# Kernel tuning notes

Measured on AMD Instinct MI355X. Metric: run time of the kernel, lower is better.

Reference implementation:

```python
import jax, jax.numpy as jnp
import numpy as np

N_HID = 18  # hardcoded hidden width in the original module


def setup_inputs() -> dict:
    key = jax.random.key(0)
    ks = jax.random.split(key, 9)
    B, NODES, F = 262144, 5, 6
    scale = 0.1
    return {
        "x": jax.random.normal(ks[0], (B, NODES, F), dtype=jnp.float32),
        "Wf": jax.random.normal(ks[1], (F, N_HID), dtype=jnp.float32) * scale,
        "bf": jnp.zeros((N_HID,), dtype=jnp.float32),
        "Wm": jax.random.normal(ks[2], (2 * N_HID, N_HID), dtype=jnp.float32) * scale,
        "bm": jnp.zeros((N_HID,), dtype=jnp.float32),
        "Wu": jax.random.normal(ks[3], (3 * N_HID, N_HID), dtype=jnp.float32) * scale,
        "bu": jnp.zeros((N_HID,), dtype=jnp.float32),
        "Wr": jax.random.normal(ks[4], (5 * N_HID, 1), dtype=jnp.float32) * scale,
        "br": jnp.zeros((1,), dtype=jnp.float32),
    }


def reference(x, Wf, bf, Wm, bm, Wu, bu, Wr, br):
    # Node feature embedding: [B,5,F] -> [B,5,18]
    h = jnp.tanh(jnp.einsum("bnf,fh->bnh", x, Wf) + bf)
    U = h  # Ua..Ue initialized to a..e
    # Ring edges (a,b),(b,c),(c,d),(d,e),(e,a): pair each node with next node
    m_in = jnp.concatenate([U, jnp.roll(U, -1, axis=1)], axis=2)  # [B,5,36]
    M = jnp.tanh(jnp.einsum("bne,eh->bnh", m_in, Wm) + bm)  # edge i = (node i, node i+1)
    # Node i is updated with message from edge (i-1, i) -> roll messages by +1
    u_in = jnp.concatenate([jnp.roll(M, 1, axis=1), U, h], axis=2)  # [B,5,54]
    U = jnp.tanh(jnp.einsum("bne,eh->bnh", u_in, Wu) + bu)
    # Readout: concat Ua..Ue -> [B,90] -> [B,1]
    flat = U.reshape(U.shape[0], 5 * N_HID)
    return flat @ Wr + br
```

## Files before the change

kernel.cpp:

```cpp
#include <hip/hip_runtime.h>
#include <stdint.h>


#define NH 18
#define PSTR 68
#define NPL 99

typedef _Float16 half8 __attribute__((ext_vector_type(8)));
typedef float float4v __attribute__((ext_vector_type(4)));
union AB { uint32_t u[4]; half8 v; };

__device__ __forceinline__ float fast_tanh(float x) {
    float t = __builtin_amdgcn_exp2f(x * 2.8853900817779268f);
    float r = __builtin_amdgcn_rcpf(t + 1.0f);
    return __builtin_fmaf(-2.0f, r, 1.0f);
}
__device__ __forceinline__ uint32_t pkh(float a, float b) {
    union { _Float16 h[2]; uint32_t u; } z;
    z.h[0] = (_Float16)a; z.h[1] = (_Float16)b; return z.u;
}

#define MFMA16(A, Bv, Cv) __builtin_amdgcn_mfma_f32_16x16x32_f16((A).v, (Bv).v, (Cv), 0, 0, 0)

__global__ __launch_bounds__(256, 4) void mp_mfma(
    const float* __restrict__ x,
    const float* __restrict__ Wf, const float* __restrict__ bf,
    const float* __restrict__ Wm, const float* __restrict__ bm,
    const float* __restrict__ Wu, const float* __restrict__ bu,
    const float* __restrict__ Wr, const float* __restrict__ br,
    float* __restrict__ out, int B)
{
    __shared__ uint32_t lds[NPL * PSTR];
    const int tid = threadIdx.x;
    const int lane = tid & 63, w = tid >> 6;
    const int l15 = lane & 15, q = lane >> 4;

    for (int v = tid; v < 640; v += 256) {
        const int fi = v >> 6, ln = v & 63;
        const int fq = ln >> 4, fl = ln & 15;
        int rt, ks, which;
        if (fi < 2)      { which = 0; rt = fi;            ks = 0; }
        else if (fi < 6) { which = 1; rt = (fi - 2) >> 1; ks = (fi - 2) & 1; }
        else             { which = 2; rt = (fi - 6) >> 1; ks = (fi - 6) & 1; }
        const int m = rt * 16 + fl;
        for (int jp = 0; jp < 4; ++jp) {
            float vv[2];
            for (int hh = 0; hh < 2; ++hh) {
                int k = ks * 32 + fq * 8 + jp * 2 + hh;
                float val = 0.0f;
                if (m < NH) {
                    if (which == 0) {
                        if (k < 6) val = Wf[k * NH + m];
                        else if (k == 6) val = bf[m];
                    } else if (which == 1) {
                        if (k < 36) val = Wm[k * NH + m];
                        else if (k == 36) val = bm[m];
                    } else {
                        if (k < NH) val = Wu[k * NH + m];
                        else if (k < 36) val = Wu[k * NH + m] + Wu[(k + NH) * NH + m];
                        else if (k == 36) val = bu[m];
                    }
                }
                vv[hh] = val;
            }
            lds[fi * 256 + ln * 4 + jp] = pkh(vv[0], vv[1]);
        }
    }
    __syncthreads();
    AB F[10];
    #pragma unroll
    for (int f = 0; f < 10; ++f) {
        const int o = f * 256 + lane * 4;
        F[f].u[0] = lds[o];     F[f].u[1] = lds[o + 1];
        F[f].u[2] = lds[o + 2]; F[f].u[3] = lds[o + 3];
    }
    __syncthreads();

    const uint32_t ONE = 0x00003C00u;
    const float4v Z = {0.f, 0.f, 0.f, 0.f};

    const int c = w * 16 + l15;
    const long long eg = (long long)blockIdx.x * 64 + c;

    uint32_t xpk[5][4];
    #pragma unroll
    for (int n = 0; n < 5; ++n) {
        xpk[n][0] = 0; xpk[n][1] = 0; xpk[n][2] = 0;
        xpk[n][3] = (q == 0) ? ONE : 0;
    }
    if (q == 0 && eg < (long long)B) {
        const float2* xp = (const float2*)x + eg * 15;
        #pragma unroll
        for (int n = 0; n < 5; ++n) {
            float2 a = xp[n * 3], b2 = xp[n * 3 + 1], d = xp[n * 3 + 2];
            xpk[n][0] = pkh(a.x, a.y); xpk[n][1] = pkh(b2.x, b2.y);
            xpk[n][2] = pkh(d.x, d.y);
        }
    }
    const int qc = q * 4 * PSTR + c;
    const int qw = q * 2 * PSTR + c;

    #pragma unroll
    for (int n = 0; n < 5; ++n) {
        AB bx; bx.u[0] = xpk[n][0]; bx.u[1] = xpk[n][1];
               bx.u[2] = xpk[n][2]; bx.u[3] = xpk[n][3];
        float4v C0 = MFMA16(F[0], bx, Z);
        float4v C1 = MFMA16(F[1], bx, Z);
        uint32_t p0 = pkh(fast_tanh(C0[0]), fast_tanh(C0[1]));
        uint32_t p1 = pkh(fast_tanh(C0[2]), fast_tanh(C0[3]));
        uint32_t p2 = pkh(fast_tanh(C1[0]), fast_tanh(C1[1]));
        const int P1 = n * 18;
        const int P2 = (n == 0) ? 81 : (n - 1) * 18 + 9;
        lds[P1 * PSTR + qw] = p0; lds[(P1 + 1) * PSTR + qw] = p1;
        lds[P2 * PSTR + qw] = p0; lds[(P2 + 1) * PSTR + qw] = p1;
        if (q == 0) { lds[(P1 + 8) * PSTR + c] = p2; lds[(P2 + 8) * PSTR + c] = p2; }
        if (n == 0) {
            lds[90 * PSTR + qw] = p0; lds[91 * PSTR + qw] = p1;
            if (q == 0) lds[98 * PSTR + c] = p2;
        }
    }

    #pragma unroll
    for (int n = 0; n < 5; ++n) {
        const int vb = n * 18;
        AB b0, b1;
        b0.u[0] = lds[vb * PSTR + qc];       b0.u[1] = lds[(vb + 1) * PSTR + qc];
        b0.u[2] = lds[(vb + 2) * PSTR + qc]; b0.u[3] = lds[(vb + 3) * PSTR + qc];
        b1.u[0] = lds[(vb + 16) * PSTR + c]; b1.u[1] = lds[(vb + 17) * PSTR + c];
        b1.u[2] = ONE; b1.u[3] = 0;
        float4v C0 = MFMA16(F[2], b0, Z); C0 = MFMA16(F[3], b1, C0);
        float4v C1 = MFMA16(F[4], b0, Z); C1 = MFMA16(F[5], b1, C1);
        uint32_t p0 = pkh(fast_tanh(C0[0]), fast_tanh(C0[1]));
        uint32_t p1 = pkh(fast_tanh(C0[2]), fast_tanh(C0[3]));
        uint32_t p2 = pkh(fast_tanh(C1[0]), fast_tanh(C1[1]));
        const int PM = n * 18 + 9;
        lds[PM * PSTR + qw] = p0; lds[(PM + 1) * PSTR + qw] = p1;
        if (q == 0) lds[(PM + 8) * PSTR + c] = p2;
    }

    float wrA[5][4], wrB[5][2];
    #pragma unroll
    for (int n = 0; n < 5; ++n) {
        #pragma unroll
        for (int r = 0; r < 4; ++r) wrA[n][r] = Wr[n * NH + q * 4 + r];
        #pragma unroll
        for (int r = 0; r < 2; ++r) wrB[n][r] = (q == 0) ? Wr[n * NH + 16 + r] : 0.0f;
    }

    float rc = 0.0f;
    #pragma unroll
    for (int n = 0; n < 5; ++n) {
        const int vb = (n == 0) ? 81 : (n - 1) * 18 + 9;
        AB b0, b1;
        b0.u[0] = lds[vb * PSTR + qc];       b0.u[1] = lds[(vb + 1) * PSTR + qc];
        b0.u[2] = lds[(vb + 2) * PSTR + qc]; b0.u[3] = lds[(vb + 3) * PSTR + qc];
        b1.u[0] = lds[(vb + 16) * PSTR + c]; b1.u[1] = lds[(vb + 17) * PSTR + c];
        b1.u[2] = ONE; b1.u[3] = 0;
        float4v C0 = MFMA16(F[6], b0, Z); C0 = MFMA16(F[7], b1, C0);
        float4v C1 = MFMA16(F[8], b0, Z); C1 = MFMA16(F[9], b1, C1);
        rc = __builtin_fmaf(fast_tanh(C0[0]), wrA[n][0], rc);
        rc = __builtin_fmaf(fast_tanh(C0[1]), wrA[n][1], rc);
        rc = __builtin_fmaf(fast_tanh(C0[2]), wrA[n][2], rc);
        rc = __builtin_fmaf(fast_tanh(C0[3]), wrA[n][3], rc);
        rc = __builtin_fmaf(fast_tanh(C1[0]), wrB[n][0], rc);
        rc = __builtin_fmaf(fast_tanh(C1[1]), wrB[n][1], rc);
    }

    float s = rc;
    s += __shfl_xor(s, 16, 64);
    s += __shfl_xor(s, 32, 64);
    if (q == 0 && eg < (long long)B) out[eg] = s + br[0];
}

extern "C" void kernel_launch(void* const* d_in, const int* in_sizes, int n_in,
                              void* d_out, int out_size, void* d_ws, size_t ws_size,
                              hipStream_t stream) {
    const float* x  = (const float*)d_in[0];
    const float* Wf = (const float*)d_in[1];
    const float* bf = (const float*)d_in[2];
    const float* Wm = (const float*)d_in[3];
    const float* bm = (const float*)d_in[4];
    const float* Wu = (const float*)d_in[5];
    const float* bu = (const float*)d_in[6];
    const float* Wr = (const float*)d_in[7];
    const float* br = (const float*)d_in[8];
    float* out = (float*)d_out;
    const int B = in_sizes[0] / 30;
    const int grid = (B + 63) / 64;
    mp_mfma<<<grid, 256, 0, stream>>>(x, Wf, bf, Wm, bm, Wu, bu, Wr, br, out, B);
}
```

Baseline: 128.1 us.

## Precompute packed fp16 weight fragments in a prep kernel, fold tanh scale into weights

Moves the per-block weight packing (with its global loads, branching and two __syncthreads) into a single-block prep kernel that writes fp16 MFMA fragments to workspace. The main kernel then loads the fragments directly from global memory. The tanh input scale is folded into the weights and biases, which removes a multiply per activation. fp16 packing now uses the cvt_pkrtz intrinsic, which rounds toward zero and slightly changes numerics. The cost is an extra kernel launch plus fragment loads through cache, in exchange for shorter setup in every one of the 4096 blocks.

```diff
diff --git a/kernel.cpp b/kernel.cpp
--- a/kernel.cpp
+++ b/kernel.cpp
@@ -5,76 +5,80 @@
 #define NH 18
 #define PSTR 68
 #define NPL 99
+#define TSCALE 2.8853900817779268f
 
 typedef _Float16 half8 __attribute__((ext_vector_type(8)));
+typedef __fp16 fp16x2 __attribute__((ext_vector_type(2)));
 typedef float float4v __attribute__((ext_vector_type(4)));
 union AB { uint32_t u[4]; half8 v; };
 
-__device__ __forceinline__ float fast_tanh(float x) {
-    float t = __builtin_amdgcn_exp2f(x * 2.8853900817779268f);
+__device__ __forceinline__ float tanh_pre(float z) {
+    float t = __builtin_amdgcn_exp2f(z);
     float r = __builtin_amdgcn_rcpf(t + 1.0f);
     return __builtin_fmaf(-2.0f, r, 1.0f);
 }
-__device__ __forceinline__ uint32_t pkh(float a, float b) {
-    union { _Float16 h[2]; uint32_t u; } z;
-    z.h[0] = (_Float16)a; z.h[1] = (_Float16)b; return z.u;
+__device__ __forceinline__ uint32_t pk2(float a, float b) {
+    union { fp16x2 h; uint32_t u; } z;
+    z.h = __builtin_amdgcn_cvt_pkrtz(a, b);
+    return z.u;
+}
+
+__global__ __launch_bounds__(640) void prep_kernel(
+    const float* __restrict__ Wf, const float* __restrict__ bf,
+    const float* __restrict__ Wm, const float* __restrict__ bm,
+    const float* __restrict__ Wu, const float* __restrict__ bu,
+    uint32_t* __restrict__ ws)
+{
+    const int tid = threadIdx.x;
+    const int fi = tid >> 6, ln = tid & 63;
+    const int fq = ln >> 4, fl = ln & 15;
+    int rt, ks, which;
+    if (fi < 2)      { which = 0; rt = fi;            ks = 0; }
+    else if (fi < 6) { which = 1; rt = (fi - 2) >> 1; ks = (fi - 2) & 1; }
+    else             { which = 2; rt = (fi - 6) >> 1; ks = (fi - 6) & 1; }
+    const int m = rt * 16 + fl;
+    for (int jp = 0; jp < 4; ++jp) {
+        float vv[2];
+        for (int hh = 0; hh < 2; ++hh) {
+            int k = ks * 32 + fq * 8 + jp * 2 + hh;
+            float val = 0.0f;
+            if (m < NH) {
+                if (which == 0) {
+                    if (k < 6) val = Wf[k * NH + m];
+                    else if (k == 6) val = bf[m];
+                } else if (which == 1) {
+                    if (k < 36) val = Wm[k * NH + m];
+                    else if (k == 36) val = bm[m];
+                } else {
+                    if (k < NH) val = Wu[k * NH + m];
+                    else if (k < 36) val = Wu[k * NH + m] + Wu[(k + NH) * NH + m];
+                    else if (k == 36) val = bu[m];
+                }
+            }
+            vv[hh] = val * TSCALE;
+        }
+        ws[fi * 256 + ln * 4 + jp] = pk2(vv[0], vv[1]);
+    }
 }
 
 #define MFMA16(A, Bv, Cv) __builtin_amdgcn_mfma_f32_16x16x32_f16((A).v, (Bv).v, (Cv), 0, 0, 0)
 
 __global__ __launch_bounds__(256, 4) void mp_mfma(
     const float* __restrict__ x,
-    const float* __restrict__ Wf, const float* __restrict__ bf,
-    const float* __restrict__ Wm, const float* __restrict__ bm,
-    const float* __restrict__ Wu, const float* __restrict__ bu,
     const float* __restrict__ Wr, const float* __restrict__ br,
-    float* __restrict__ out, int B)
+    const uint32_t* __restrict__ ws, float* __restrict__ out, int B)
 {
     __shared__ uint32_t lds[NPL * PSTR];
     const int tid = threadIdx.x;
     const int lane = tid & 63, w = tid >> 6;
     const int l15 = lane & 15, q = lane >> 4;
 
-    for (int v = tid; v < 640; v += 256) {
-        const int fi = v >> 6, ln = v & 63;
-        const int fq = ln >> 4, fl = ln & 15;
-        int rt, ks, which;
-        if (fi < 2)      { which = 0; rt = fi;            ks = 0; }
-        else if (fi < 6) { which = 1; rt = (fi - 2) >> 1; ks = (fi - 2) & 1; }
-        else             { which = 2; rt = (fi - 6) >> 1; ks = (fi - 6) & 1; }
-        const int m = rt * 16 + fl;
-        for (int jp = 0; jp < 4; ++jp) {
-            float vv[2];
-            for (int hh = 0; hh < 2; ++hh) {
-                int k = ks * 32 + fq * 8 + jp * 2 + hh;
-                float val = 0.0f;
-                if (m < NH) {
-                    if (which == 0) {
-                        if (k < 6) val = Wf[k * NH + m];
-                        else if (k == 6) val = bf[m];
-                    } else if (which == 1) {
-                        if (k < 36) val = Wm[k * NH + m];
-                        else if (k == 36) val = bm[m];
-                    } else {
-                        if (k < NH) val = Wu[k * NH + m];
-                        else if (k < 36) val = Wu[k * NH + m] + Wu[(k + NH) * NH + m];
-                        else if (k == 36) val = bu[m];
-                    }
-                }
-                vv[hh] = val;
-            }
-            lds[fi * 256 + ln * 4 + jp] = pkh(vv[0], vv[1]);
-        }
-    }
-    __syncthreads();
     AB F[10];
     #pragma unroll
     for (int f = 0; f < 10; ++f) {
-        const int o = f * 256 + lane * 4;
-        F[f].u[0] = lds[o];     F[f].u[1] = lds[o + 1];
-        F[f].u[2] = lds[o + 2]; F[f].u[3] = lds[o + 3];
+        const uint32_t* p = ws + f * 256 + lane * 4;
+        F[f].u[0] = p[0]; F[f].u[1] = p[1]; F[f].u[2] = p[2]; F[f].u[3] = p[3];
     }
-    __syncthreads();
 
     const uint32_t ONE = 0x00003C00u;
     const float4v Z = {0.f, 0.f, 0.f, 0.f};
@@ -93,8 +97,8 @@
         #pragma unroll
         for (int n = 0; n < 5; ++n) {
             float2 a = xp[n * 3], b2 = xp[n * 3 + 1], d = xp[n * 3 + 2];
-            xpk[n][0] = pkh(a.x, a.y); xpk[n][1] = pkh(b2.x, b2.y);
-            xpk[n][2] = pkh(d.x, d.y);
+            xpk[n][0] = pk2(a.x, a.y); xpk[n][1] = pk2(b2.x, b2.y);
+            xpk[n][2] = pk2(d.x, d.y);
         }
     }
     const int qc = q * 4 * PSTR + c;
@@ -106,9 +110,9 @@
                bx.u[2] = xpk[n][2]; bx.u[3] = xpk[n][3];
         float4v C0 = MFMA16(F[0], bx, Z);
         float4v C1 = MFMA16(F[1], bx, Z);
-        uint32_t p0 = pkh(fast_tanh(C0[0]), fast_tanh(C0[1]));
-        uint32_t p1 = pkh(fast_tanh(C0[2]), fast_tanh(C0[3]));
-        uint32_t p2 = pkh(fast_tanh(C1[0]), fast_tanh(C1[1]));
+        uint32_t p0 = pk2(tanh_pre(C0[0]), tanh_pre(C0[1]));
+        uint32_t p1 = pk2(tanh_pre(C0[2]), tanh_pre(C0[3]));
+        uint32_t p2 = pk2(tanh_pre(C1[0]), tanh_pre(C1[1]));
         const int P1 = n * 18;
         const int P2 = (n == 0) ? 81 : (n - 1) * 18 + 9;
         lds[P1 * PSTR + qw] = p0; lds[(P1 + 1) * PSTR + qw] = p1;
@@ -130,9 +134,9 @@
         b1.u[2] = ONE; b1.u[3] = 0;
         float4v C0 = MFMA16(F[2], b0, Z); C0 = MFMA16(F[3], b1, C0);
         float4v C1 = MFMA16(F[4], b0, Z); C1 = MFMA16(F[5], b1, C1);
-        uint32_t p0 = pkh(fast_tanh(C0[0]), fast_tanh(C0[1]));
-        uint32_t p1 = pkh(fast_tanh(C0[2]), fast_tanh(C0[3]));
-        uint32_t p2 = pkh(fast_tanh(C1[0]), fast_tanh(C1[1]));
+        uint32_t p0 = pk2(tanh_pre(C0[0]), tanh_pre(C0[1]));
+        uint32_t p1 = pk2(tanh_pre(C0[2]), tanh_pre(C0[3]));
+        uint32_t p2 = pk2(tanh_pre(C1[0]), tanh_pre(C1[1]));
         const int PM = n * 18 + 9;
         lds[PM * PSTR + qw] = p0; lds[(PM + 1) * PSTR + qw] = p1;
         if (q == 0) lds[(PM + 8) * PSTR + c] = p2;
@@ -158,12 +162,12 @@
         b1.u[2] = ONE; b1.u[3] = 0;
         float4v C0 = MFMA16(F[6], b0, Z); C0 = MFMA16(F[7], b1, C0);
         float4v C1 = MFMA16(F[8], b0, Z); C1 = MFMA16(F[9], b1, C1);
-        rc = __builtin_fmaf(fast_tanh(C0[0]), wrA[n][0], rc);
-        rc = __builtin_fmaf(fast_tanh(C0[1]), wrA[n][1], rc);
-        rc = __builtin_fmaf(fast_tanh(C0[2]), wrA[n][2], rc);
-        rc = __builtin_fmaf(fast_tanh(C0[3]), wrA[n][3], rc);
-        rc = __builtin_fmaf(fast_tanh(C1[0]), wrB[n][0], rc);
-        rc = __builtin_fmaf(fast_tanh(C1[1]), wrB[n][1], rc);
+        rc = __builtin_fmaf(tanh_pre(C0[0]), wrA[n][0], rc);
+        rc = __builtin_fmaf(tanh_pre(C0[1]), wrA[n][1], rc);
+        rc = __builtin_fmaf(tanh_pre(C0[2]), wrA[n][2], rc);
+        rc = __builtin_fmaf(tanh_pre(C0[3]), wrA[n][3], rc);
+        rc = __builtin_fmaf(tanh_pre(C1[0]), wrB[n][0], rc);
+        rc = __builtin_fmaf(tanh_pre(C1[1]), wrB[n][1], rc);
     }
 
     float s = rc;
@@ -186,6 +190,9 @@
     const float* br = (const float*)d_in[8];
     float* out = (float*)d_out;
     const int B = in_sizes[0] / 30;
+
+    uint32_t* ws = (uint32_t*)d_ws;
+    prep_kernel<<<1, 640, 0, stream>>>(Wf, bf, Wm, bm, Wu, bu, ws);
     const int grid = (B + 63) / 64;
-    mp_mfma<<<grid, 256, 0, stream>>>(x, Wf, bf, Wm, bm, Wu, bu, Wr, br, out, B);
+    mp_mfma<<<grid, 256, 0, stream>>>(x, Wr, br, ws, out, B);
 }
```

New measurement: 111.1 us. 13.3% less time.
